# Optimization experiments

Hardware: AMD Instinct MI355X
Metric: run time of the kernel (lower is better)

## Reference

```python
import jax, jax.numpy as jnp
import numpy as np

B, S, D, H, F = 2, 2048, 3072, 32, 8192
DH = D // H  # 96
EPS = 1e-5


def setup_inputs() -> dict:
    key = jax.random.key(0)
    ks = jax.random.split(key, 16)
    sd = 0.02
    inp = {
        "hidden_states": jax.random.normal(ks[0], (B, S, D), jnp.float32),
        "ln1_g": jnp.ones((D,), jnp.float32),
        "ln1_b": jnp.zeros((D,), jnp.float32),
        "Wq": jax.random.normal(ks[1], (D, H, DH), jnp.float32) * sd,
        "bq": jnp.zeros((H, DH), jnp.float32),
        "Wk": jax.random.normal(ks[2], (D, H, DH), jnp.float32) * sd,
        "bk": jnp.zeros((H, DH), jnp.float32),
        "Wv": jax.random.normal(ks[3], (D, H, DH), jnp.float32) * sd,
        "bv": jnp.zeros((H, DH), jnp.float32),
        "Wo": jax.random.normal(ks[4], (H, DH, D), jnp.float32) * sd,
        "bo": jnp.zeros((D,), jnp.float32),
        "ln2_g": jnp.ones((D,), jnp.float32),
        "ln2_b": jnp.zeros((D,), jnp.float32),
        "W1": jax.random.normal(ks[5], (D, F), jnp.float32) * sd,
        "b1": jnp.zeros((F,), jnp.float32),
        "W2": jax.random.normal(ks[6], (F, D), jnp.float32) * sd,
        "b2": jnp.zeros((D,), jnp.float32),
    }
    return inp


def _layernorm(x, g, b):
    m = jnp.mean(x, axis=-1, keepdims=True)
    v = jnp.mean(jnp.square(x - m), axis=-1, keepdims=True)
    return (x - m) * jax.lax.rsqrt(v + EPS) * g + b


def reference(hidden_states, ln1_g, ln1_b, Wq, bq, Wk, bk, Wv, bv, Wo, bo,
              ln2_g, ln2_b, W1, b1, W2, b2):
    # --- LN + self-attention + residual ---
    h = _layernorm(hidden_states, ln1_g, ln1_b)  # [B,S,D]
    q = jnp.einsum('bsd,dhk->bshk', h, Wq) + bq  # [B,S,H,DH]
    k = jnp.einsum('bsd,dhk->bshk', h, Wk) + bk
    v = jnp.einsum('bsd,dhk->bshk', h, Wv) + bv
    scale = 1.0 / np.sqrt(DH).astype(np.float32)
    scores = jnp.einsum('bshk,bthk->bhst', q, k) * scale  # [B,H,S,S]
    attn = jax.nn.softmax(scores, axis=-1)
    ctx = jnp.einsum('bhst,bthk->bshk', attn, v)  # [B,S,H,DH]
    attn_out = jnp.einsum('bshk,hkd->bsd', ctx, Wo) + bo
    h1 = hidden_states + attn_out
    # --- LN + MLP + residual ---
    h2 = _layernorm(h1, ln2_g, ln2_b)
    mlp = jax.nn.gelu(h2 @ W1 + b1, approximate=False) @ W2 + b2
    return h1 + mlp
```

## Files before the change

### kernel.cpp

```cpp
#include <hip/hip_runtime.h>
#include <math.h>

#define DEV __device__ __forceinline__

typedef __attribute__((ext_vector_type(8))) __bf16 bfrag;
typedef __attribute__((ext_vector_type(4))) float f4;
typedef __attribute__((ext_vector_type(8))) unsigned short u16x8;
typedef __attribute__((ext_vector_type(4))) unsigned short u16x4;

DEV unsigned short f2bf(float f) {
  unsigned u = __float_as_uint(f);
  u += 0x7fff + ((u >> 16) & 1);
  return (unsigned short)(u >> 16);
}

DEV void gload_lds16(const void* g, void* l) {
  __builtin_amdgcn_global_load_lds((const __attribute__((address_space(1))) void*)g,
                                   (__attribute__((address_space(3))) void*)l, 16, 0, 0);
}

template<int EPI, int OUTBF>
__global__ __launch_bounds__(256, 2)
void gemm_bt(const unsigned short* __restrict__ A,
             const unsigned short* __restrict__ Bt,
             const float* __restrict__ bias,
             const float* __restrict__ res,
             void* __restrict__ outp,
             int M, int N, int K)
{
  __shared__ unsigned short As[2][128 * 32];
  __shared__ unsigned short Bs[2][128 * 32];
  const int tid = threadIdx.x;
  const int lane = tid & 63;
  const int wid = tid >> 6;
  const int wr = wid >> 1, wc = wid & 1;
  const int l15 = lane & 15, lg = lane >> 4;
  const long tM = (long)blockIdx.x * 128;
  const long tN = (long)blockIdx.y * 128;

  const int c0 = tid, c1 = tid + 256;
  const int r0 = c0 >> 2, k0 = (c0 & 3) * 8;
  const int r1 = c1 >> 2, k1 = (c1 & 3) * 8;

  const unsigned short* A0 = A + (tM + r0) * (long)K + k0;
  const unsigned short* A1 = A + (tM + r1) * (long)K + k1;
  const unsigned short* B0 = Bt + (tN + r0) * (long)K + k0;
  const unsigned short* B1 = Bt + (tN + r1) * (long)K + k1;

  auto stage = [&](int kt, int buf) {
    const long ko = (long)kt * 32;
    gload_lds16(A0 + ko, &As[buf][c0 * 8]);
    gload_lds16(A1 + ko, &As[buf][c1 * 8]);
    gload_lds16(B0 + ko, &Bs[buf][c0 * 8]);
    gload_lds16(B1 + ko, &Bs[buf][c1 * 8]);
  };

  stage(0, 0);
  f4 acc[4][4] = {};
  const int nk = K >> 5;
  int cur = 0;
  __syncthreads();
  for (int kt = 0; kt < nk; ++kt) {
    if (kt + 1 < nk) stage(kt + 1, cur ^ 1);
    bfrag aF[4], bF[4];
#pragma unroll
    for (int m = 0; m < 4; ++m)
      aF[m] = *(const bfrag*)&As[cur][(wr * 64 + m * 16 + l15) * 32 + lg * 8];
#pragma unroll
    for (int n = 0; n < 4; ++n)
      bF[n] = *(const bfrag*)&Bs[cur][(wc * 64 + n * 16 + l15) * 32 + lg * 8];
#pragma unroll
    for (int m = 0; m < 4; ++m)
#pragma unroll
      for (int n = 0; n < 4; ++n)
        acc[m][n] = __builtin_amdgcn_mfma_f32_16x16x32_bf16(aF[m], bF[n], acc[m][n], 0, 0, 0);
    __syncthreads();
    cur ^= 1;
  }

#pragma unroll
  for (int m = 0; m < 4; ++m) {
#pragma unroll
    for (int n = 0; n < 4; ++n) {
      const long col = tN + wc * 64 + n * 16 + l15;
      const float bv = bias[col];
#pragma unroll
      for (int e = 0; e < 4; ++e) {
        const long row = tM + wr * 64 + m * 16 + lg * 4 + e;
        float v = acc[m][n][e] + bv;
        if (EPI == 1) v = 0.5f * v * (1.0f + erff(v * 0.70710678118654752f));
        if (EPI == 2) v += res[row * N + col];
        if (OUTBF) ((unsigned short*)outp)[row * N + col] = f2bf(v);
        else       ((float*)outp)[row * N + col] = v;
      }
    }
  }
}

__global__ __launch_bounds__(256)
void ln_bf16(const float* __restrict__ x, const float* __restrict__ g,
             const float* __restrict__ b, unsigned short* __restrict__ out)
{
  __shared__ float red[4];
  const int tid = threadIdx.x;
  const long row = blockIdx.x;
  const float* xr = x + row * 3072;
  float4 v[3];
  float s = 0.f;
#pragma unroll
  for (int i = 0; i < 3; ++i) {
    v[i] = *(const float4*)&xr[i * 1024 + tid * 4];
    s += v[i].x + v[i].y + v[i].z + v[i].w;
  }
#pragma unroll
  for (int o = 32; o > 0; o >>= 1) s += __shfl_xor(s, o);
  if ((tid & 63) == 0) red[tid >> 6] = s;
  __syncthreads();
  s = red[0] + red[1] + red[2] + red[3];
  const float mean = s * (1.f / 3072.f);
  float vs = 0.f;
#pragma unroll
  for (int i = 0; i < 3; ++i) {
    const float dx = v[i].x - mean, dy = v[i].y - mean;
    const float dz = v[i].z - mean, dw = v[i].w - mean;
    vs += dx * dx + dy * dy + dz * dz + dw * dw;
  }
#pragma unroll
  for (int o = 32; o > 0; o >>= 1) vs += __shfl_xor(vs, o);
  __syncthreads();
  if ((tid & 63) == 0) red[tid >> 6] = vs;
  __syncthreads();
  vs = red[0] + red[1] + red[2] + red[3];
  const float rstd = rsqrtf(vs * (1.f / 3072.f) + 1e-5f);
#pragma unroll
  for (int i = 0; i < 3; ++i) {
    const int idx = i * 1024 + tid * 4;
    const float* vp = (const float*)&v[i];
    u16x4 o4;
#pragma unroll
    for (int c = 0; c < 4; ++c)
      o4[c] = f2bf((vp[c] - mean) * rstd * g[idx + c] + b[idx + c]);
    *(u16x4*)&out[row * 3072 + idx] = o4;
  }
}

__global__ __launch_bounds__(256)
void transpose_f32_bf16(const float* __restrict__ in, unsigned short* __restrict__ out,
                        int R, int C)
{
  __shared__ float tile[32][33];
  const int tx = threadIdx.x & 31, ty = threadIdx.x >> 5;
  const long r0 = (long)blockIdx.y * 32, cc0 = (long)blockIdx.x * 32;
#pragma unroll
  for (int i = 0; i < 4; ++i)
    tile[ty + 8 * i][tx] = in[(r0 + ty + 8 * i) * C + cc0 + tx];
  __syncthreads();
#pragma unroll
  for (int i = 0; i < 4; ++i)
    out[(cc0 + ty + 8 * i) * R + r0 + tx] = f2bf(tile[tx][ty + 8 * i]);
}

__global__ __launch_bounds__(256, 2)
void attn_fwd(const unsigned short* __restrict__ qg,
              const unsigned short* __restrict__ kg,
              const unsigned short* __restrict__ vg,
              unsigned short* __restrict__ ctx)
{
  __shared__ unsigned short Qs[64 * 104];
  __shared__ unsigned short Ks[64 * 104];
  __shared__ unsigned short Vt[96 * 80];
  __shared__ unsigned short Ps[4 * 16 * 72];
  const int tid = threadIdx.x;
  const int lane = tid & 63;
  const int w = tid >> 6;
  const int l15 = lane & 15, lg = lane >> 4;
  const int bid = blockIdx.x;
  const int qb = bid & 31;
  const int h = (bid >> 5) & 31;
  const int b = bid >> 10;
  const long base = ((long)b * 2048) * 3072 + h * 96;
  const int qbase = qb * 64;

#pragma unroll
  for (int i = 0; i < 3; ++i) {
    const int c = tid + i * 256;
    const int r = c / 12, c8 = (c % 12) * 8;
    *(u16x8*)&Qs[r * 104 + c8] = *(const u16x8*)&qg[base + (long)(qbase + r) * 3072 + c8];
  }

  float m_run = -1e30f, l_run = 0.f;
  f4 O[6] = {};
  const float sc = 0.1020620726f * 1.4426950409f;

  for (int t = 0; t < 32; ++t) {
    __syncthreads();
    const int kb = t * 64;
#pragma unroll
    for (int i = 0; i < 3; ++i) {
      const int c = tid + i * 256;
      const int r = c / 12, c8 = (c % 12) * 8;
      *(u16x8*)&Ks[r * 104 + c8] = *(const u16x8*)&kg[base + (long)(kb + r) * 3072 + c8];
      const u16x8 vv = *(const u16x8*)&vg[base + (long)(kb + r) * 3072 + c8];
#pragma unroll
      for (int j = 0; j < 8; ++j)
        Vt[(c8 + j) * 80 + r] = vv[j];
    }
    __syncthreads();

    f4 sf[4];
#pragma unroll
    for (int mb = 0; mb < 4; ++mb) {
      f4 z = {0.f, 0.f, 0.f, 0.f};
      sf[mb] = z;
#pragma unroll
      for (int ks = 0; ks < 3; ++ks) {
        bfrag kf = *(const bfrag*)&Ks[(mb * 16 + l15) * 104 + ks * 32 + lg * 8];
        bfrag qf = *(const bfrag*)&Qs[(w * 16 + l15) * 104 + ks * 32 + lg * 8];
        sf[mb] = __builtin_amdgcn_mfma_f32_16x16x32_bf16(kf, qf, sf[mb], 0, 0, 0);
      }
    }
    float p[16];
    float tmax = -1e30f;
#pragma unroll
    for (int mb = 0; mb < 4; ++mb)
#pragma unroll
      for (int e = 0; e < 4; ++e) {
        const float sv = sf[mb][e] * sc;
        p[mb * 4 + e] = sv;
        tmax = fmaxf(tmax, sv);
      }
    tmax = fmaxf(tmax, __shfl_xor(tmax, 16));
    tmax = fmaxf(tmax, __shfl_xor(tmax, 32));
    const float mnew = fmaxf(m_run, tmax);
    const float alpha = exp2f(m_run - mnew);
    float psum = 0.f;
#pragma unroll
    for (int i = 0; i < 16; ++i) {
      p[i] = exp2f(p[i] - mnew);
      psum += p[i];
    }
    psum += __shfl_xor(psum, 16);
    psum += __shfl_xor(psum, 32);
    l_run = l_run * alpha + psum;
    m_run = mnew;
#pragma unroll
    for (int mb = 0; mb < 4; ++mb) {
      u16x4 pw;
#pragma unroll
      for (int e = 0; e < 4; ++e) pw[e] = f2bf(p[mb * 4 + e]);
      *(u16x4*)&Ps[w * 1152 + l15 * 72 + mb * 16 + lg * 4] = pw;
    }
    float aE[4];
#pragma unroll
    for (int e = 0; e < 4; ++e) aE[e] = __shfl(alpha, lg * 4 + e);
#pragma unroll
    for (int nb = 0; nb < 6; ++nb)
#pragma unroll
      for (int e = 0; e < 4; ++e) O[nb][e] *= aE[e];
#pragma unroll
    for (int nb = 0; nb < 6; ++nb)
#pragma unroll
      for (int ks = 0; ks < 2; ++ks) {
        bfrag pf = *(const bfrag*)&Ps[w * 1152 + l15 * 72 + ks * 32 + lg * 8];
        bfrag vf = *(const bfrag*)&Vt[(nb * 16 + l15) * 80 + ks * 32 + lg * 8];
        O[nb] = __builtin_amdgcn_mfma_f32_16x16x32_bf16(pf, vf, O[nb], 0, 0, 0);
      }
  }
  float lE[4];
#pragma unroll
  for (int e = 0; e < 4; ++e) lE[e] = 1.f / __shfl(l_run, lg * 4 + e);
#pragma unroll
  for (int nb = 0; nb < 6; ++nb)
#pragma unroll
    for (int e = 0; e < 4; ++e) {
      const long row = qbase + w * 16 + lg * 4 + e;
      ctx[base + row * 3072 + nb * 16 + l15] = f2bf(O[nb][e] * lE[e]);
    }
}

extern "C" void kernel_launch(void* const* d_in, const int* in_sizes, int n_in,
                              void* d_out, int out_size, void* d_ws, size_t ws_size,
                              hipStream_t stream)
{
  (void)in_sizes; (void)n_in; (void)out_size; (void)ws_size;
  const float* x    = (const float*)d_in[0];
  const float* ln1g = (const float*)d_in[1];
  const float* ln1b = (const float*)d_in[2];
  const float* Wq   = (const float*)d_in[3];
  const float* bq   = (const float*)d_in[4];
  const float* Wk   = (const float*)d_in[5];
  const float* bk   = (const float*)d_in[6];
  const float* Wv   = (const float*)d_in[7];
  const float* bv   = (const float*)d_in[8];
  const float* Wo   = (const float*)d_in[9];
  const float* bo   = (const float*)d_in[10];
  const float* ln2g = (const float*)d_in[11];
  const float* ln2b = (const float*)d_in[12];
  const float* W1   = (const float*)d_in[13];
  const float* b1   = (const float*)d_in[14];
  const float* W2   = (const float*)d_in[15];
  const float* b2   = (const float*)d_in[16];

  char* ws = (char*)d_ws;
  unsigned short* WqT = (unsigned short*)(ws + 0);
  unsigned short* WkT = (unsigned short*)(ws + 18874368);
  unsigned short* WvT = (unsigned short*)(ws + 37748736);
  unsigned short* WoT = (unsigned short*)(ws + 56623104);
  unsigned short* W1T = (unsigned short*)(ws + 75497472);
  unsigned short* W2T = (unsigned short*)(ws + 125829120);
  unsigned short* hbf  = (unsigned short*)(ws + 176160768);
  unsigned short* ctxb = hbf;
  unsigned short* qb_  = (unsigned short*)(ws + 201326592);
  unsigned short* h2   = qb_;
  unsigned short* kb_  = (unsigned short*)(ws + 226492416);
  unsigned short* act  = kb_;
  unsigned short* vb_  = (unsigned short*)(ws + 293601280);
  float*          h1   = (float*)(ws + 318767104);

  const dim3 blk(256);

  transpose_f32_bf16<<<dim3(96, 96),  blk, 0, stream>>>(Wq, WqT, 3072, 3072);
  transpose_f32_bf16<<<dim3(96, 96),  blk, 0, stream>>>(Wk, WkT, 3072, 3072);
  transpose_f32_bf16<<<dim3(96, 96),  blk, 0, stream>>>(Wv, WvT, 3072, 3072);
  transpose_f32_bf16<<<dim3(96, 96),  blk, 0, stream>>>(Wo, WoT, 3072, 3072);
  transpose_f32_bf16<<<dim3(256, 96), blk, 0, stream>>>(W1, W1T, 3072, 8192);
  transpose_f32_bf16<<<dim3(96, 256), blk, 0, stream>>>(W2, W2T, 8192, 3072);

  ln_bf16<<<4096, blk, 0, stream>>>(x, ln1g, ln1b, hbf);

  gemm_bt<0, 1><<<dim3(32, 24), blk, 0, stream>>>(hbf, WqT, bq, nullptr, qb_, 4096, 3072, 3072);
  gemm_bt<0, 1><<<dim3(32, 24), blk, 0, stream>>>(hbf, WkT, bk, nullptr, kb_, 4096, 3072, 3072);
  gemm_bt<0, 1><<<dim3(32, 24), blk, 0, stream>>>(hbf, WvT, bv, nullptr, vb_, 4096, 3072, 3072);

  attn_fwd<<<2048, blk, 0, stream>>>(qb_, kb_, vb_, ctxb);

  gemm_bt<2, 0><<<dim3(32, 24), blk, 0, stream>>>(ctxb, WoT, bo, x, h1, 4096, 3072, 3072);

  ln_bf16<<<4096, blk, 0, stream>>>(h1, ln2g, ln2b, h2);

  gemm_bt<1, 1><<<dim3(32, 64), blk, 0, stream>>>(h2, W1T, b1, nullptr, act, 4096, 8192, 3072);
  gemm_bt<2, 0><<<dim3(32, 24), blk, 0, stream>>>(act, W2T, b2, h1, (float*)d_out, 4096, 3072, 8192);
}
```

Measured before the change: 1.434 ms.

## Produce V transposed from GEMM and load it directly in attention

```diff
diff --git a/kernel.cpp b/kernel.cpp
--- a/kernel.cpp
+++ b/kernel.cpp
@@ -19,7 +19,7 @@
                                    (__attribute__((address_space(3))) void*)l, 16, 0, 0);
 }
 
-template<int EPI, int OUTBF>
+template<int EPI, int OUTBF, int BIASROW>
 __global__ __launch_bounds__(256, 2)
 void gemm_bt(const unsigned short* __restrict__ A,
              const unsigned short* __restrict__ Bt,
@@ -83,11 +83,11 @@
 #pragma unroll
     for (int n = 0; n < 4; ++n) {
       const long col = tN + wc * 64 + n * 16 + l15;
-      const float bv = bias[col];
+      const float bcol = BIASROW ? 0.f : bias[col];
 #pragma unroll
       for (int e = 0; e < 4; ++e) {
         const long row = tM + wr * 64 + m * 16 + lg * 4 + e;
-        float v = acc[m][n][e] + bv;
+        float v = acc[m][n][e] + (BIASROW ? bias[row] : bcol);
         if (EPI == 1) v = 0.5f * v * (1.0f + erff(v * 0.70710678118654752f));
         if (EPI == 2) v += res[row * N + col];
         if (OUTBF) ((unsigned short*)outp)[row * N + col] = f2bf(v);
@@ -160,25 +160,26 @@
     out[(cc0 + ty + 8 * i) * R + r0 + tx] = f2bf(tile[tx][ty + 8 * i]);
 }
 
-__global__ __launch_bounds__(256, 2)
+__global__ __launch_bounds__(256, 3)
 void attn_fwd(const unsigned short* __restrict__ qg,
               const unsigned short* __restrict__ kg,
-              const unsigned short* __restrict__ vg,
+              const unsigned short* __restrict__ vT,
               unsigned short* __restrict__ ctx)
 {
   __shared__ unsigned short Qs[64 * 104];
   __shared__ unsigned short Ks[64 * 104];
-  __shared__ unsigned short Vt[96 * 80];
+  __shared__ unsigned short Vt[96 * 72];
   __shared__ unsigned short Ps[4 * 16 * 72];
   const int tid = threadIdx.x;
   const int lane = tid & 63;
   const int w = tid >> 6;
   const int l15 = lane & 15, lg = lane >> 4;
-  const int bid = blockIdx.x;
+  const int bid = (blockIdx.x & 7) * 256 + (blockIdx.x >> 3);
   const int qb = bid & 31;
   const int h = (bid >> 5) & 31;
   const int b = bid >> 10;
   const long base = ((long)b * 2048) * 3072 + h * 96;
+  const long vbase = (long)(h * 96) * 4096 + (long)b * 2048;
   const int qbase = qb * 64;
 
 #pragma unroll
@@ -200,10 +201,12 @@
       const int c = tid + i * 256;
       const int r = c / 12, c8 = (c % 12) * 8;
       *(u16x8*)&Ks[r * 104 + c8] = *(const u16x8*)&kg[base + (long)(kb + r) * 3072 + c8];
-      const u16x8 vv = *(const u16x8*)&vg[base + (long)(kb + r) * 3072 + c8];
-#pragma unroll
-      for (int j = 0; j < 8; ++j)
-        Vt[(c8 + j) * 80 + r] = vv[j];
+    }
+#pragma unroll
+    for (int i = 0; i < 3; ++i) {
+      const int idx = tid + i * 256;
+      const int d = idx >> 3, c8 = (idx & 7) * 8;
+      *(u16x8*)&Vt[d * 72 + c8] = *(const u16x8*)&vT[vbase + (long)d * 4096 + kb + c8];
     }
     __syncthreads();
 
@@ -262,7 +265,7 @@
 #pragma unroll
       for (int ks = 0; ks < 2; ++ks) {
         bfrag pf = *(const bfrag*)&Ps[w * 1152 + l15 * 72 + ks * 32 + lg * 8];
-        bfrag vf = *(const bfrag*)&Vt[(nb * 16 + l15) * 80 + ks * 32 + lg * 8];
+        bfrag vf = *(const bfrag*)&Vt[(nb * 16 + l15) * 72 + ks * 32 + lg * 8];
         O[nb] = __builtin_amdgcn_mfma_f32_16x16x32_bf16(pf, vf, O[nb], 0, 0, 0);
       }
   }
@@ -328,16 +331,16 @@
 
   ln_bf16<<<4096, blk, 0, stream>>>(x, ln1g, ln1b, hbf);
 
-  gemm_bt<0, 1><<<dim3(32, 24), blk, 0, stream>>>(hbf, WqT, bq, nullptr, qb_, 4096, 3072, 3072);
-  gemm_bt<0, 1><<<dim3(32, 24), blk, 0, stream>>>(hbf, WkT, bk, nullptr, kb_, 4096, 3072, 3072);
-  gemm_bt<0, 1><<<dim3(32, 24), blk, 0, stream>>>(hbf, WvT, bv, nullptr, vb_, 4096, 3072, 3072);
+  gemm_bt<0, 1, 0><<<dim3(32, 24), blk, 0, stream>>>(hbf, WqT, bq, nullptr, qb_, 4096, 3072, 3072);
+  gemm_bt<0, 1, 0><<<dim3(32, 24), blk, 0, stream>>>(hbf, WkT, bk, nullptr, kb_, 4096, 3072, 3072);
+  gemm_bt<0, 1, 1><<<dim3(24, 32), blk, 0, stream>>>(WvT, hbf, bv, nullptr, vb_, 3072, 4096, 3072);
 
   attn_fwd<<<2048, blk, 0, stream>>>(qb_, kb_, vb_, ctxb);
 
-  gemm_bt<2, 0><<<dim3(32, 24), blk, 0, stream>>>(ctxb, WoT, bo, x, h1, 4096, 3072, 3072);
+  gemm_bt<2, 0, 0><<<dim3(32, 24), blk, 0, stream>>>(ctxb, WoT, bo, x, h1, 4096, 3072, 3072);
 
   ln_bf16<<<4096, blk, 0, stream>>>(h1, ln2g, ln2b, h2);
 
-  gemm_bt<1, 1><<<dim3(32, 64), blk, 0, stream>>>(h2, W1T, b1, nullptr, act, 4096, 8192, 3072);
-  gemm_bt<2, 0><<<dim3(32, 24), blk, 0, stream>>>(act, W2T, b2, h1, (float*)d_out, 4096, 3072, 8192);
-}
+  gemm_bt<1, 1, 0><<<dim3(32, 64), blk, 0, stream>>>(h2, W1T, b1, nullptr, act, 4096, 8192, 3072);
+  gemm_bt<2, 0, 0><<<dim3(32, 24), blk, 0, stream>>>(act, W2T, b2, h1, (float*)d_out, 4096, 3072, 8192);
+}
```

Measured after the change: 1.250 ms. -12.8%, faster.
